# Kernel tuning notes

Measured on AMD Instinct MI355X. Metric: run time of the kernel, lower is better.

The kernel has to match this reference:

```python
import jax, jax.numpy as jnp
import numpy as np

B, N, K, H, C = 16, 2048, 9, 128, 2  # K = nb_neighbors, kernel_size = K+1


def setup_inputs() -> dict:
    key = jax.random.key(0)
    ks = jax.random.split(key, 7)
    s = 0.1
    x = jax.random.normal(ks[0], (B, N, C), jnp.float32)
    Wconv = jax.random.normal(ks[1], (H, C, K + 1), jnp.float32) * s  # conv1d weight
    bconv = jax.random.normal(ks[2], (H,), jnp.float32) * s
    W1 = jax.random.normal(ks[3], (H, C), jnp.float32) * s
    b1 = jax.random.normal(ks[4], (H,), jnp.float32) * s
    W2 = jax.random.normal(ks[5], (H, H), jnp.float32) * s
    b2 = jax.random.normal(ks[6], (H,), jnp.float32) * s
    return {"x": x, "Wconv": Wconv, "bconv": bconv, "W1": W1, "b1": b1, "W2": W2, "b2": b2}


def reference(x, Wconv, bconv, W1, b1, W2, b2):
    # node embedding: W1(x)
    node_emb = jnp.einsum('bnc,hc->bnh', x, W1) + b1  # (B,N,H)

    # pairwise Euclidean distances (B,N,N) via the GEMM form
    sq = jnp.sum(x * x, axis=-1)  # (B,N)
    d2 = sq[:, :, None] + sq[:, None, :] - 2.0 * jnp.einsum('bnc,bmc->bnm', x, x)
    dist = jnp.sqrt(jnp.maximum(d2, 0.0))

    # torch: topk(k=N) (descending) then take last K+1 columns -> the K+1
    # smallest distances ordered descending (nearest/self last)
    knn = jnp.flip(jnp.argsort(dist, axis=-1)[..., : K + 1], axis=-1)  # (B,N,K+1)

    # batched gather of neighbor coords: (B,N,K+1,C)
    coords = jax.vmap(lambda xb, ib: xb[ib])(x, knn)

    # conv1d with kernel spanning the full window -> single output position,
    # i.e. a contraction over (channel, position)
    conv_emb = jnp.einsum('bnkc,hck->bnh', coords, Wconv) + bconv  # (B,N,H)
    conv_emb = jnp.einsum('bnh,eh->bne', conv_emb, W2) + b2

    return node_emb + conv_emb
```

## Files before the change

kernel.cpp:

```cpp
#include <hip/hip_runtime.h>
#include <cfloat>
#include <stdint.h>

#define B_   16
#define N_   2048
#define KK   10
#define H_   128
#define SUB  32
#define NCH  (N_ / SUB)

#define RANK_BLOCKS (B_ * 32)
#define WEFF_OUT    (H_ * KK * 2 + H_)
#define WEFF_BLOCKS ((WEFF_OUT * 4) / 256)

__device__ inline uint32_t f32_ordered(float f) {
    uint32_t u = __float_as_uint(f);
    return (u & 0x80000000u) ? ~u : (u | 0x80000000u);
}

__global__ __launch_bounds__(256) void setup_kernel(
    const float* __restrict__ x,
    const float* __restrict__ Wconv, const float* __restrict__ bconv,
    const float* __restrict__ b1,    const float* __restrict__ W2,
    const float* __restrict__ b2,
    float4* __restrict__ xsorted,
    float*  __restrict__ weff,
    float*  __restrict__ btot)
{
#pragma clang fp contract(off)
    __shared__ __align__(16) uint64_t sk[N_];
    __shared__ int pcnt[4 * 64];
    const int tid = threadIdx.x;

    if (blockIdx.x >= RANK_BLOCKS) {
        const int g = (blockIdx.x - RANK_BLOCKS) * 256 + tid;
        const int o = g >> 2, q = g & 3;
        float acc = 0.f;
        if (o < H_ * KK * 2) {
            const int e = o / 20, r = o % 20, k = r >> 1, c = r & 1;
            const float* w2p = W2 + e * H_ + q * 32;
            const float* wcp = Wconv + (q * 32) * (2 * KK) + c * KK + k;
#pragma unroll 8
            for (int h = 0; h < 32; ++h)
                acc += w2p[h] * wcp[h * (2 * KK)];
        } else {
            const int e = o - H_ * KK * 2;
            const float* w2p = W2 + e * H_ + q * 32;
            const float* bcp = bconv + q * 32;
#pragma unroll 8
            for (int h = 0; h < 32; ++h) acc += w2p[h] * bcp[h];
        }
        acc += __shfl_xor(acc, 1, 64);
        acc += __shfl_xor(acc, 2, 64);
        if (q == 0) {
            if (o < H_ * KK * 2) weff[o] = acc;
            else {
                const int e = o - H_ * KK * 2;
                btot[e] = acc + b1[e] + b2[e];
            }
        }
        return;
    }

    const int b  = blockIdx.x >> 5;
    const int sg = blockIdx.x & 31;
    const float2* xb = (const float2*)(x + (size_t)b * N_ * 2);

    for (int i = tid; i < N_; i += 256)
        sk[i] = ((uint64_t)f32_ordered(xb[i].x) << 32) | (uint32_t)i;
    __syncthreads();

    const int el = tid & 63;
    const int pt = tid >> 6;
    const uint64_t kown = sk[sg * 64 + el];
    const ulonglong2* sk2 = (const ulonglong2*)sk + pt * 256;
    int cnt = 0;
#pragma unroll 2
    for (int j = 0; j < 256; j += 4) {
        ulonglong2 t0 = sk2[j + 0];
        ulonglong2 t1 = sk2[j + 1];
        ulonglong2 t2 = sk2[j + 2];
        ulonglong2 t3 = sk2[j + 3];
        cnt += (int)(t0.x < kown) + (int)(t0.y < kown)
             + (int)(t1.x < kown) + (int)(t1.y < kown)
             + (int)(t2.x < kown) + (int)(t2.y < kown)
             + (int)(t3.x < kown) + (int)(t3.y < kown);
    }
    pcnt[pt * 64 + el] = cnt;
    __syncthreads();

    if (tid < 64) {
        const int r = pcnt[tid] + pcnt[64 + tid] + pcnt[128 + tid] + pcnt[192 + tid];
        const int i = sg * 64 + tid;
        float2 p = xb[i];
        float sm = p.x * p.x + p.y * p.y;
        xsorted[(size_t)b * N_ + r] =
            make_float4(p.x, p.y, sm, __uint_as_float((uint32_t)i));
    }
}

__global__ __launch_bounds__(512, 4) void knn_conv_kernel(
    const float4* __restrict__ xsorted,
    const float* __restrict__ W1,
    const float* __restrict__ weff,
    const float* __restrict__ btot,
    float* __restrict__ out)
{
#pragma clang fp contract(off)
    __shared__ float4 xs4[N_];
    __shared__ float  wcoord[64 * 21];

    const int tid  = threadIdx.x;
    const int w    = tid >> 6;
    const int r    = tid & 7;
    const int qm   = tid >> 3;
    const int b    = blockIdx.x >> 5;
    const int tile = blockIdx.x & 31;

    const float4* xb = xsorted + (size_t)b * N_;
    for (int i = tid; i < N_; i += 512) xs4[i] = xb[i];
    __syncthreads();

    const float4 qv = xs4[tile * 64 + qm];
    const float  qx = qv.x, qy = qv.y, sqn = qv.z;
    const int    gfirst = tile * 64 + w * 8;
    const float  qa  = xs4[gfirst].x;
    const float  qbx = xs4[gfirst + 7].x;

    const uint64_t KINIT = (((uint64_t)0x7F7FFFFFu) << 32) | 0x3FFFFFu;
    uint64_t hk[KK];
#pragma unroll
    for (int j = 0; j < KK; ++j) hk[j] = KINIT;
    float h9d  = FLT_MAX;
    float shb  = FLT_MAX;
    float gate = FLT_MAX;

    auto insert = [&](float dc, float cw, int m) {
        uint32_t oi = __float_as_uint(cw);
        uint64_t key = ((uint64_t)__float_as_uint(dc) << 32)
                     | (oi << 11) | (uint32_t)m;
        if (key < hk[KK - 1]) {
#pragma unroll
            for (int j = KK - 1; j >= 1; --j) {
                bool cj  = key < hk[j];
                bool cjm = key < hk[j - 1];
                hk[j] = cj ? (cjm ? hk[j - 1] : key) : hk[j];
            }
            hk[0] = (key < hk[0]) ? key : hk[0];
        }
        h9d  = __uint_as_float((uint32_t)(hk[KK - 1] >> 32));
        gate = fminf(h9d, shb);
    };

    auto scan_chunk = [&](int mc) {
        const int m0 = mc + r;
        float4 c0 = xs4[m0 + 0];
        float4 c1 = xs4[m0 + 8];
        float4 c2 = xs4[m0 + 16];
        float4 c3 = xs4[m0 + 24];
        float dc0, dc1, dc2, dc3;
        { float s = sqn + c0.z; float pr = qx * c0.x;
          float dt = __builtin_fmaf(qy, c0.y, pr);
          float d2 = __builtin_fmaf(-2.0f, dt, s); dc0 = d2 > 0.0f ? d2 : 0.0f; }
        { float s = sqn + c1.z; float pr = qx * c1.x;
          float dt = __builtin_fmaf(qy, c1.y, pr);
          float d2 = __builtin_fmaf(-2.0f, dt, s); dc1 = d2 > 0.0f ? d2 : 0.0f; }
        { float s = sqn + c2.z; float pr = qx * c2.x;
          float dt = __builtin_fmaf(qy, c2.y, pr);
          float d2 = __builtin_fmaf(-2.0f, dt, s); dc2 = d2 > 0.0f ? d2 : 0.0f; }
        { float s = sqn + c3.z; float pr = qx * c3.x;
          float dt = __builtin_fmaf(qy, c3.y, pr);
          float d2 = __builtin_fmaf(-2.0f, dt, s); dc3 = d2 > 0.0f ? d2 : 0.0f; }
        if (dc0 <= gate) insert(dc0, c0.w, m0 + 0);
        if (dc1 <= gate) insert(dc1, c1.w, m0 + 8);
        if (dc2 <= gate) insert(dc2, c2.w, m0 + 16);
        if (dc3 <= gate) insert(dc3, c3.w, m0 + 24);
    };

    auto bounds = [&]() {
        float gb = h9d;
        gb = fminf(gb, __shfl_xor(gb, 1, 64));
        gb = fminf(gb, __shfl_xor(gb, 2, 64));
        gb = fminf(gb, __shfl_xor(gb, 4, 64));
        shb = gb; gate = fminf(h9d, gb);
        float wm = gb;
        wm = fmaxf(wm, __shfl_xor(wm, 8,  64));
        wm = fmaxf(wm, __shfl_xor(wm, 16, 64));
        wm = fmaxf(wm, __shfl_xor(wm, 32, 64));
        return wm;
    };

    const int home = tile * 2 + (w >> 2);
    int c0s = home - 1;
    if (c0s < 0) c0s = 0;
    if (c0s > NCH - 3) c0s = NCH - 3;
    scan_chunk((c0s + 0) * SUB);
    scan_chunk((c0s + 1) * SUB);
    scan_chunk((c0s + 2) * SUB);

    int  cl = c0s - 1, cr = c0s + 3;
    bool la = (cl >= 0), ra = (cr <= NCH - 1);
    while (la || ra) {
        float wm = bounds();
        if (la) {
            float gl = qa - xs4[cl * SUB + SUB - 1].x;
            if (__builtin_fmaf(gl, gl, -4e-6f) > wm) la = false;
            else { scan_chunk(cl * SUB); cl -= 1; la = (cl >= 0); }
        }
        if (ra) {
            float gr = xs4[cr * SUB].x - qbx;
            if (__builtin_fmaf(gr, gr, -4e-6f) > wm) ra = false;
            else { scan_chunk(cr * SUB); cr += 1; ra = (cr <= NCH - 1); }
        }
    }

    const int e = tid & 127;
    float we[20];
    {
        const float4* wp = (const float4*)(weff + e * 20);
#pragma unroll
        for (int rr = 0; rr < 5; ++rr) {
            float4 v = wp[rr];
            we[4 * rr + 0] = v.x; we[4 * rr + 1] = v.y;
            we[4 * rr + 2] = v.z; we[4 * rr + 3] = v.w;
        }
    }
    const float w1x = W1[e * 2 + 0];
    const float w1y = W1[e * 2 + 1];
    const float bt  = btot[e];

    {
#pragma unroll
        for (int sel = 0; sel < KK; ++sel) {
            uint64_t v  = hk[0];
            uint64_t t1 = __shfl_xor((unsigned long long)v, 1, 64);
            uint64_t m1 = v  < t1 ? v  : t1;
            uint64_t t2 = __shfl_xor((unsigned long long)m1, 2, 64);
            uint64_t m2 = m1 < t2 ? m1 : t2;
            uint64_t t4 = __shfl_xor((unsigned long long)m2, 4, 64);
            uint64_t vm = m2 < t4 ? m2 : t4;
            if (v == vm) {
#pragma unroll
                for (int j = 0; j < KK - 1; ++j) hk[j] = hk[j + 1];
                hk[KK - 1] = 0xFFFFFFFFFFFFFFFFull;
                float4 c = xs4[(int)(vm & 0x7FF)];
                const int k = (KK - 1) - sel;
                wcoord[qm * 21 + 2 * k + 0] = c.x;
                wcoord[qm * 21 + 2 * k + 1] = c.y;
            }
        }
    }
    __syncthreads();

    const int qb_ = tid >> 7;
    const size_t obase = (size_t)b * N_ * H_;
#pragma unroll
    for (int jj = 0; jj < 16; ++jj) {
        const int qq = qb_ + 4 * jj;
        float4 xq = xs4[tile * 64 + qq];
        uint32_t orig = __float_as_uint(xq.w);
        const float* wc = &wcoord[qq * 21];
        float acc = bt;
        acc += xq.x * w1x;
        acc += xq.y * w1y;
#pragma unroll
        for (int k = 0; k < KK; ++k) {
            acc += wc[2 * k + 0] * we[2 * k + 0];
            acc += wc[2 * k + 1] * we[2 * k + 1];
        }
        out[obase + (size_t)orig * H_ + e] = acc;
    }
}

extern "C" void kernel_launch(void* const* d_in, const int* in_sizes, int n_in,
                              void* d_out, int out_size, void* d_ws, size_t ws_size,
                              hipStream_t stream) {
    const float* x     = (const float*)d_in[0];
    const float* Wconv = (const float*)d_in[1];
    const float* bconv = (const float*)d_in[2];
    const float* W1    = (const float*)d_in[3];
    const float* b1    = (const float*)d_in[4];
    const float* W2    = (const float*)d_in[5];
    const float* b2    = (const float*)d_in[6];
    float* out  = (float*)d_out;
    float* weff = (float*)d_ws;
    float* btot = weff + H_ * KK * 2;
    float4* xsorted = (float4*)((char*)d_ws + 16384);

    setup_kernel<<<dim3(RANK_BLOCKS + WEFF_BLOCKS), dim3(256), 0, stream>>>(
        x, Wconv, bconv, b1, W2, b2, xsorted, weff, btot);
    knn_conv_kernel<<<dim3(B_ * (N_ / 64)), dim3(512), 0, stream>>>(
        xsorted, W1, weff, btot, out);
}
```

Before: 150.9 us.

## Process one query per wavefront with ballot-based shared top-K insertion

```diff
diff --git a/kernel.cpp b/kernel.cpp
--- a/kernel.cpp
+++ b/kernel.cpp
@@ -6,8 +6,6 @@
 #define N_   2048
 #define KK   10
 #define H_   128
-#define SUB  32
-#define NCH  (N_ / SUB)
 
 #define RANK_BLOCKS (B_ * 32)
 #define WEFF_OUT    (H_ * KK * 2 + H_)
@@ -112,8 +110,7 @@
 
     const int tid  = threadIdx.x;
     const int w    = tid >> 6;
-    const int r    = tid & 7;
-    const int qm   = tid >> 3;
+    const int lane = tid & 63;
     const int b    = blockIdx.x >> 5;
     const int tile = blockIdx.x & 31;
 
@@ -121,96 +118,96 @@
     for (int i = tid; i < N_; i += 512) xs4[i] = xb[i];
     __syncthreads();
 
-    const float4 qv = xs4[tile * 64 + qm];
-    const float  qx = qv.x, qy = qv.y, sqn = qv.z;
-    const int    gfirst = tile * 64 + w * 8;
-    const float  qa  = xs4[gfirst].x;
-    const float  qbx = xs4[gfirst + 7].x;
-
     const uint64_t KINIT = (((uint64_t)0x7F7FFFFFu) << 32) | 0x3FFFFFu;
-    uint64_t hk[KK];
-#pragma unroll
-    for (int j = 0; j < KK; ++j) hk[j] = KINIT;
-    float h9d  = FLT_MAX;
-    float shb  = FLT_MAX;
-    float gate = FLT_MAX;
-
-    auto insert = [&](float dc, float cw, int m) {
-        uint32_t oi = __float_as_uint(cw);
-        uint64_t key = ((uint64_t)__float_as_uint(dc) << 32)
-                     | (oi << 11) | (uint32_t)m;
-        if (key < hk[KK - 1]) {
-#pragma unroll
-            for (int j = KK - 1; j >= 1; --j) {
-                bool cj  = key < hk[j];
-                bool cjm = key < hk[j - 1];
-                hk[j] = cj ? (cjm ? hk[j - 1] : key) : hk[j];
-            }
-            hk[0] = (key < hk[0]) ? key : hk[0];
-        }
-        h9d  = __uint_as_float((uint32_t)(hk[KK - 1] >> 32));
-        gate = fminf(h9d, shb);
-    };
-
-    auto scan_chunk = [&](int mc) {
-        const int m0 = mc + r;
-        float4 c0 = xs4[m0 + 0];
-        float4 c1 = xs4[m0 + 8];
-        float4 c2 = xs4[m0 + 16];
-        float4 c3 = xs4[m0 + 24];
-        float dc0, dc1, dc2, dc3;
-        { float s = sqn + c0.z; float pr = qx * c0.x;
-          float dt = __builtin_fmaf(qy, c0.y, pr);
-          float d2 = __builtin_fmaf(-2.0f, dt, s); dc0 = d2 > 0.0f ? d2 : 0.0f; }
-        { float s = sqn + c1.z; float pr = qx * c1.x;
-          float dt = __builtin_fmaf(qy, c1.y, pr);
-          float d2 = __builtin_fmaf(-2.0f, dt, s); dc1 = d2 > 0.0f ? d2 : 0.0f; }
-        { float s = sqn + c2.z; float pr = qx * c2.x;
-          float dt = __builtin_fmaf(qy, c2.y, pr);
-          float d2 = __builtin_fmaf(-2.0f, dt, s); dc2 = d2 > 0.0f ? d2 : 0.0f; }
-        { float s = sqn + c3.z; float pr = qx * c3.x;
-          float dt = __builtin_fmaf(qy, c3.y, pr);
-          float d2 = __builtin_fmaf(-2.0f, dt, s); dc3 = d2 > 0.0f ? d2 : 0.0f; }
-        if (dc0 <= gate) insert(dc0, c0.w, m0 + 0);
-        if (dc1 <= gate) insert(dc1, c1.w, m0 + 8);
-        if (dc2 <= gate) insert(dc2, c2.w, m0 + 16);
-        if (dc3 <= gate) insert(dc3, c3.w, m0 + 24);
-    };
-
-    auto bounds = [&]() {
-        float gb = h9d;
-        gb = fminf(gb, __shfl_xor(gb, 1, 64));
-        gb = fminf(gb, __shfl_xor(gb, 2, 64));
-        gb = fminf(gb, __shfl_xor(gb, 4, 64));
-        shb = gb; gate = fminf(h9d, gb);
-        float wm = gb;
-        wm = fmaxf(wm, __shfl_xor(wm, 8,  64));
-        wm = fmaxf(wm, __shfl_xor(wm, 16, 64));
-        wm = fmaxf(wm, __shfl_xor(wm, 32, 64));
-        return wm;
-    };
-
-    const int home = tile * 2 + (w >> 2);
-    int c0s = home - 1;
-    if (c0s < 0) c0s = 0;
-    if (c0s > NCH - 3) c0s = NCH - 3;
-    scan_chunk((c0s + 0) * SUB);
-    scan_chunk((c0s + 1) * SUB);
-    scan_chunk((c0s + 2) * SUB);
-
-    int  cl = c0s - 1, cr = c0s + 3;
-    bool la = (cl >= 0), ra = (cr <= NCH - 1);
-    while (la || ra) {
-        float wm = bounds();
-        if (la) {
-            float gl = qa - xs4[cl * SUB + SUB - 1].x;
-            if (__builtin_fmaf(gl, gl, -4e-6f) > wm) la = false;
-            else { scan_chunk(cl * SUB); cl -= 1; la = (cl >= 0); }
-        }
-        if (ra) {
-            float gr = xs4[cr * SUB].x - qbx;
-            if (__builtin_fmaf(gr, gr, -4e-6f) > wm) ra = false;
-            else { scan_chunk(cr * SUB); cr += 1; ra = (cr <= NCH - 1); }
+
+    float gate_seed = FLT_MAX;
+    float pqx = 0.f, pqy = 0.f;
+    float ps9 = FLT_MAX;
+
+    for (int j = 0; j < 8; ++j) {
+        const int p = tile * 64 + w * 8 + j;
+        const float4 qv = xs4[p];
+        const float qx = qv.x, qy = qv.y, sqn = qv.z;
+
+        float gate;
+        if (j == 0) gate = FLT_MAX;
+        else {
+            float dx = qx - pqx, dy = qy - pqy;
+            float dq2 = dx * dx + dy * dy;
+            float t = sqrtf(ps9) + sqrtf(dq2);
+            gate = __builtin_fmaf(t * t, 1.0005f, 1e-6f);
+        }
+
+        uint64_t s_list = KINIT;
+        int  le = p, re = p;
+        bool ld = false, rd = false;
+
+        while (!ld || !rd) {
+            const bool left = (lane < 32);
+            const int  m    = left ? (le - 32 + lane) : (re + lane - 32);
+            const bool sok  = left ? !ld : !rd;
+            const bool valid = sok && (m >= 0) && (m < N_);
+            const int  mc   = valid ? m : 0;
+            float4 c4 = xs4[mc];
+            float s  = sqn + c4.z;
+            float pr = qx * c4.x;
+            float dt = __builtin_fmaf(qy, c4.y, pr);
+            float d2 = __builtin_fmaf(-2.0f, dt, s);
+            float dc = d2 > 0.0f ? d2 : 0.0f;
+            const bool acc = valid && (dc <= gate);
+
+            unsigned long long mask = __ballot(acc);
+            if (mask) {
+                const uint32_t oi = __float_as_uint(c4.w);
+                const uint64_t key = ((uint64_t)__float_as_uint(dc) << 32)
+                                   | (oi << 11) | (uint32_t)mc;
+                do {
+                    const int i = (int)__builtin_ctzll(mask);
+                    mask &= mask - 1;
+                    const uint64_t v =
+                        (uint64_t)__shfl((unsigned long long)key, i, 64);
+                    unsigned long long bl = __ballot(s_list < v);
+                    const int pos = (int)__popcll(bl & 0x3FFull);
+                    const uint64_t sp =
+                        (uint64_t)__shfl_up((unsigned long long)s_list, 1, 64);
+                    s_list = (lane == pos) ? v : ((lane > pos) ? sp : s_list);
+                } while (mask);
+            }
+
+            const uint64_t s9 =
+                (uint64_t)__shfl((unsigned long long)s_list, 9, 64);
+            const float s9d = __uint_as_float((uint32_t)(s9 >> 32));
+            gate = fminf(gate, s9d);
+
+            le -= 32; re += 32;
+            if (!ld) {
+                if (le <= 0) ld = true;
+                else {
+                    float gl = qx - xs4[le - 1].x;
+                    if (__builtin_fmaf(gl, gl, -4e-6f) > s9d) ld = true;
+                }
+            }
+            if (!rd) {
+                if (re >= N_) rd = true;
+                else {
+                    float gr = xs4[re].x - qx;
+                    if (__builtin_fmaf(gr, gr, -4e-6f) > s9d) rd = true;
+                }
+            }
+        }
+
+        if (lane < KK) {
+            float4 c = xs4[(int)(s_list & 0x7FF)];
+            const int qloc = w * 8 + j;
+            wcoord[qloc * 21 + 2 * (KK - 1 - lane) + 0] = c.x;
+            wcoord[qloc * 21 + 2 * (KK - 1 - lane) + 1] = c.y;
+        }
+
+        {
+            const uint64_t s9 =
+                (uint64_t)__shfl((unsigned long long)s_list, 9, 64);
+            ps9 = __uint_as_float((uint32_t)(s9 >> 32));
+            pqx = qx; pqy = qy;
         }
     }
 
@@ -228,28 +225,6 @@
     const float w1x = W1[e * 2 + 0];
     const float w1y = W1[e * 2 + 1];
     const float bt  = btot[e];
-
-    {
-#pragma unroll
-        for (int sel = 0; sel < KK; ++sel) {
-            uint64_t v  = hk[0];
-            uint64_t t1 = __shfl_xor((unsigned long long)v, 1, 64);
-            uint64_t m1 = v  < t1 ? v  : t1;
-            uint64_t t2 = __shfl_xor((unsigned long long)m1, 2, 64);
-            uint64_t m2 = m1 < t2 ? m1 : t2;
-            uint64_t t4 = __shfl_xor((unsigned long long)m2, 4, 64);
-            uint64_t vm = m2 < t4 ? m2 : t4;
-            if (v == vm) {
-#pragma unroll
-                for (int j = 0; j < KK - 1; ++j) hk[j] = hk[j + 1];
-                hk[KK - 1] = 0xFFFFFFFFFFFFFFFFull;
-                float4 c = xs4[(int)(vm & 0x7FF)];
-                const int k = (KK - 1) - sel;
-                wcoord[qm * 21 + 2 * k + 0] = c.x;
-                wcoord[qm * 21 + 2 * k + 1] = c.y;
-            }
-        }
-    }
     __syncthreads();
 
     const int qb_ = tid >> 7;
```

Result: slower. 189.1 us (+25.3%).

## Merge per-lane KNN heaps after initial scan to tighten pruning bound; skip final merge

Applied to the files above, without the earlier changes.

```diff
diff --git a/kernel.cpp b/kernel.cpp
--- a/kernel.cpp
+++ b/kernel.cpp
@@ -99,6 +99,84 @@
     }
 }
 
+#define D2C(c4v, dcv) { float s_ = sqn + (c4v).z; float pr_ = qx * (c4v).x; \
+    float dt_ = __builtin_fmaf(qy, (c4v).y, pr_); \
+    float d2_ = __builtin_fmaf(-2.0f, dt_, s_); (dcv) = d2_ > 0.0f ? d2_ : 0.0f; }
+
+#define INSERT(dcv, cwv, mv) do { \
+    uint64_t key_ = ((uint64_t)__float_as_uint(dcv) << 32) \
+                  | (__float_as_uint(cwv) << 11) | (uint32_t)(mv); \
+    if (key_ < h9) { \
+        bool c0_ = key_ < h0, c1_ = key_ < h1, c2_ = key_ < h2; \
+        bool c3_ = key_ < h3, c4_ = key_ < h4, c5_ = key_ < h5; \
+        bool c6_ = key_ < h6, c7_ = key_ < h7, c8_ = key_ < h8; \
+        h9 = c8_ ? h8 : key_; \
+        h8 = c8_ ? (c7_ ? h7 : key_) : h8; \
+        h7 = c7_ ? (c6_ ? h6 : key_) : h7; \
+        h6 = c6_ ? (c5_ ? h5 : key_) : h6; \
+        h5 = c5_ ? (c4_ ? h4 : key_) : h5; \
+        h4 = c4_ ? (c3_ ? h3 : key_) : h4; \
+        h3 = c3_ ? (c2_ ? h2 : key_) : h3; \
+        h2 = c2_ ? (c1_ ? h1 : key_) : h2; \
+        h1 = c1_ ? (c0_ ? h0 : key_) : h1; \
+        h0 = c0_ ? key_ : h0; \
+        h9d  = __uint_as_float((uint32_t)(h9 >> 32)); \
+        gate = fminf(h9d, shb); \
+        pins = true; \
+    } \
+} while (0)
+
+#define SCAN_CHUNK(mcv) do { \
+    const int m0_ = (mcv) + r; \
+    float4 ca_ = xs4[m0_ + 0]; \
+    float4 cb_ = xs4[m0_ + 8]; \
+    float4 cc_ = xs4[m0_ + 16]; \
+    float4 cd_ = xs4[m0_ + 24]; \
+    float da_, db_, dc_, dd_; \
+    D2C(ca_, da_); D2C(cb_, db_); D2C(cc_, dc_); D2C(cd_, dd_); \
+    if (da_ <= gate) INSERT(da_, ca_.w, m0_ + 0); \
+    if (db_ <= gate) INSERT(db_, cb_.w, m0_ + 8); \
+    if (dc_ <= gate) INSERT(dc_, cc_.w, m0_ + 16); \
+    if (dd_ <= gate) INSERT(dd_, cd_.w, m0_ + 24); \
+} while (0)
+
+#define BOUNDS(wmv) do { \
+    float gb_ = h9d; \
+    gb_ = fminf(gb_, __shfl_xor(gb_, 1, 64)); \
+    gb_ = fminf(gb_, __shfl_xor(gb_, 2, 64)); \
+    gb_ = fminf(gb_, __shfl_xor(gb_, 4, 64)); \
+    float hb_ = __uint_as_float((uint32_t)(h1 >> 32)); \
+    hb_ = fmaxf(hb_, __shfl_xor(hb_, 1, 64)); \
+    hb_ = fmaxf(hb_, __shfl_xor(hb_, 2, 64)); \
+    hb_ = fmaxf(hb_, __shfl_xor(hb_, 4, 64)); \
+    shb  = fminf(shb, fminf(gb_, hb_)); \
+    gate = fminf(h9d, shb); \
+    float wm_ = shb; \
+    wm_ = fmaxf(wm_, __shfl_xor(wm_, 8,  64)); \
+    wm_ = fmaxf(wm_, __shfl_xor(wm_, 16, 64)); \
+    wm_ = fmaxf(wm_, __shfl_xor(wm_, 32, 64)); \
+    (wmv) = wm_; \
+} while (0)
+
+#define SELSTEP(selv, A0,A1,A2,A3,A4,A5,A6,A7,A8,A9) do { \
+    uint64_t v_ = A0; \
+    uint64_t x_ = (uint64_t)__shfl_xor((unsigned long long)v_, 1, 64); \
+    uint64_t m_ = v_ < x_ ? v_ : x_; \
+    x_ = (uint64_t)__shfl_xor((unsigned long long)m_, 2, 64); \
+    m_ = m_ < x_ ? m_ : x_; \
+    x_ = (uint64_t)__shfl_xor((unsigned long long)m_, 4, 64); \
+    m_ = m_ < x_ ? m_ : x_; \
+    if (v_ == m_) { A0=A1; A1=A2; A2=A3; A3=A4; A4=A5; A5=A6; A6=A7; A7=A8; A8=A9; \
+                    A9 = 0xFFFFFFFFFFFFFFFFull; } \
+    if (r == 0) { \
+        float4 c_ = xs4[(int)(m_ & 0x7FF)]; \
+        const int k_ = (KK - 1) - (selv); \
+        wcoord[qm * 21 + 2 * k_ + 0] = c_.x; \
+        wcoord[qm * 21 + 2 * k_ + 1] = c_.y; \
+    } \
+    lastv = m_; \
+} while (0)
+
 __global__ __launch_bounds__(512, 4) void knn_conv_kernel(
     const float4* __restrict__ xsorted,
     const float* __restrict__ W1,
@@ -128,89 +206,54 @@
     const float  qbx = xs4[gfirst + 7].x;
 
     const uint64_t KINIT = (((uint64_t)0x7F7FFFFFu) << 32) | 0x3FFFFFu;
-    uint64_t hk[KK];
-#pragma unroll
-    for (int j = 0; j < KK; ++j) hk[j] = KINIT;
+    uint64_t h0 = KINIT, h1 = KINIT, h2 = KINIT, h3 = KINIT, h4 = KINIT;
+    uint64_t h5 = KINIT, h6 = KINIT, h7 = KINIT, h8 = KINIT, h9 = KINIT;
     float h9d  = FLT_MAX;
     float shb  = FLT_MAX;
     float gate = FLT_MAX;
-
-    auto insert = [&](float dc, float cw, int m) {
-        uint32_t oi = __float_as_uint(cw);
-        uint64_t key = ((uint64_t)__float_as_uint(dc) << 32)
-                     | (oi << 11) | (uint32_t)m;
-        if (key < hk[KK - 1]) {
-#pragma unroll
-            for (int j = KK - 1; j >= 1; --j) {
-                bool cj  = key < hk[j];
-                bool cjm = key < hk[j - 1];
-                hk[j] = cj ? (cjm ? hk[j - 1] : key) : hk[j];
-            }
-            hk[0] = (key < hk[0]) ? key : hk[0];
-        }
-        h9d  = __uint_as_float((uint32_t)(hk[KK - 1] >> 32));
-        gate = fminf(h9d, shb);
-    };
-
-    auto scan_chunk = [&](int mc) {
-        const int m0 = mc + r;
-        float4 c0 = xs4[m0 + 0];
-        float4 c1 = xs4[m0 + 8];
-        float4 c2 = xs4[m0 + 16];
-        float4 c3 = xs4[m0 + 24];
-        float dc0, dc1, dc2, dc3;
-        { float s = sqn + c0.z; float pr = qx * c0.x;
-          float dt = __builtin_fmaf(qy, c0.y, pr);
-          float d2 = __builtin_fmaf(-2.0f, dt, s); dc0 = d2 > 0.0f ? d2 : 0.0f; }
-        { float s = sqn + c1.z; float pr = qx * c1.x;
-          float dt = __builtin_fmaf(qy, c1.y, pr);
-          float d2 = __builtin_fmaf(-2.0f, dt, s); dc1 = d2 > 0.0f ? d2 : 0.0f; }
-        { float s = sqn + c2.z; float pr = qx * c2.x;
-          float dt = __builtin_fmaf(qy, c2.y, pr);
-          float d2 = __builtin_fmaf(-2.0f, dt, s); dc2 = d2 > 0.0f ? d2 : 0.0f; }
-        { float s = sqn + c3.z; float pr = qx * c3.x;
-          float dt = __builtin_fmaf(qy, c3.y, pr);
-          float d2 = __builtin_fmaf(-2.0f, dt, s); dc3 = d2 > 0.0f ? d2 : 0.0f; }
-        if (dc0 <= gate) insert(dc0, c0.w, m0 + 0);
-        if (dc1 <= gate) insert(dc1, c1.w, m0 + 8);
-        if (dc2 <= gate) insert(dc2, c2.w, m0 + 16);
-        if (dc3 <= gate) insert(dc3, c3.w, m0 + 24);
-    };
-
-    auto bounds = [&]() {
-        float gb = h9d;
-        gb = fminf(gb, __shfl_xor(gb, 1, 64));
-        gb = fminf(gb, __shfl_xor(gb, 2, 64));
-        gb = fminf(gb, __shfl_xor(gb, 4, 64));
-        shb = gb; gate = fminf(h9d, gb);
-        float wm = gb;
-        wm = fmaxf(wm, __shfl_xor(wm, 8,  64));
-        wm = fmaxf(wm, __shfl_xor(wm, 16, 64));
-        wm = fmaxf(wm, __shfl_xor(wm, 32, 64));
-        return wm;
-    };
+    bool  pins = false;
 
     const int home = tile * 2 + (w >> 2);
     int c0s = home - 1;
     if (c0s < 0) c0s = 0;
     if (c0s > NCH - 3) c0s = NCH - 3;
-    scan_chunk((c0s + 0) * SUB);
-    scan_chunk((c0s + 1) * SUB);
-    scan_chunk((c0s + 2) * SUB);
+    SCAN_CHUNK((c0s + 0) * SUB);
+    SCAN_CHUNK((c0s + 1) * SUB);
+    SCAN_CHUNK((c0s + 2) * SUB);
+
+    uint64_t lastv = 0;
+    {
+        uint64_t t0 = h0, t1 = h1, t2 = h2, t3 = h3, t4 = h4;
+        uint64_t t5 = h5, t6 = h6, t7 = h7, t8 = h8, t9 = h9;
+        SELSTEP(0, t0,t1,t2,t3,t4,t5,t6,t7,t8,t9);
+        SELSTEP(1, t0,t1,t2,t3,t4,t5,t6,t7,t8,t9);
+        SELSTEP(2, t0,t1,t2,t3,t4,t5,t6,t7,t8,t9);
+        SELSTEP(3, t0,t1,t2,t3,t4,t5,t6,t7,t8,t9);
+        SELSTEP(4, t0,t1,t2,t3,t4,t5,t6,t7,t8,t9);
+        SELSTEP(5, t0,t1,t2,t3,t4,t5,t6,t7,t8,t9);
+        SELSTEP(6, t0,t1,t2,t3,t4,t5,t6,t7,t8,t9);
+        SELSTEP(7, t0,t1,t2,t3,t4,t5,t6,t7,t8,t9);
+        SELSTEP(8, t0,t1,t2,t3,t4,t5,t6,t7,t8,t9);
+        SELSTEP(9, t0,t1,t2,t3,t4,t5,t6,t7,t8,t9);
+        shb  = __uint_as_float((uint32_t)(lastv >> 32));
+        gate = fminf(h9d, shb);
+    }
+    pins = false;
 
     int  cl = c0s - 1, cr = c0s + 3;
     bool la = (cl >= 0), ra = (cr <= NCH - 1);
     while (la || ra) {
-        float wm = bounds();
+        float wm;
+        BOUNDS(wm);
         if (la) {
             float gl = qa - xs4[cl * SUB + SUB - 1].x;
             if (__builtin_fmaf(gl, gl, -4e-6f) > wm) la = false;
-            else { scan_chunk(cl * SUB); cl -= 1; la = (cl >= 0); }
+            else { SCAN_CHUNK(cl * SUB); cl -= 1; la = (cl >= 0); }
         }
         if (ra) {
             float gr = xs4[cr * SUB].x - qbx;
             if (__builtin_fmaf(gr, gr, -4e-6f) > wm) ra = false;
-            else { scan_chunk(cr * SUB); cr += 1; ra = (cr <= NCH - 1); }
+            else { SCAN_CHUNK(cr * SUB); cr += 1; ra = (cr <= NCH - 1); }
         }
     }
 
@@ -229,26 +272,17 @@
     const float w1y = W1[e * 2 + 1];
     const float bt  = btot[e];
 
-    {
-#pragma unroll
-        for (int sel = 0; sel < KK; ++sel) {
-            uint64_t v  = hk[0];
-            uint64_t t1 = __shfl_xor((unsigned long long)v, 1, 64);
-            uint64_t m1 = v  < t1 ? v  : t1;
-            uint64_t t2 = __shfl_xor((unsigned long long)m1, 2, 64);
-            uint64_t m2 = m1 < t2 ? m1 : t2;
-            uint64_t t4 = __shfl_xor((unsigned long long)m2, 4, 64);
-            uint64_t vm = m2 < t4 ? m2 : t4;
-            if (v == vm) {
-#pragma unroll
-                for (int j = 0; j < KK - 1; ++j) hk[j] = hk[j + 1];
-                hk[KK - 1] = 0xFFFFFFFFFFFFFFFFull;
-                float4 c = xs4[(int)(vm & 0x7FF)];
-                const int k = (KK - 1) - sel;
-                wcoord[qm * 21 + 2 * k + 0] = c.x;
-                wcoord[qm * 21 + 2 * k + 1] = c.y;
-            }
-        }
+    if (__ballot(pins)) {
+        SELSTEP(0, h0,h1,h2,h3,h4,h5,h6,h7,h8,h9);
+        SELSTEP(1, h0,h1,h2,h3,h4,h5,h6,h7,h8,h9);
+        SELSTEP(2, h0,h1,h2,h3,h4,h5,h6,h7,h8,h9);
+        SELSTEP(3, h0,h1,h2,h3,h4,h5,h6,h7,h8,h9);
+        SELSTEP(4, h0,h1,h2,h3,h4,h5,h6,h7,h8,h9);
+        SELSTEP(5, h0,h1,h2,h3,h4,h5,h6,h7,h8,h9);
+        SELSTEP(6, h0,h1,h2,h3,h4,h5,h6,h7,h8,h9);
+        SELSTEP(7, h0,h1,h2,h3,h4,h5,h6,h7,h8,h9);
+        SELSTEP(8, h0,h1,h2,h3,h4,h5,h6,h7,h8,h9);
+        SELSTEP(9, h0,h1,h2,h3,h4,h5,h6,h7,h8,h9);
     }
     __syncthreads();
 
```

After: 146.2 us. -3.1%, faster.
